# Performance work log

Hardware: AMD Instinct MI355X
Metric: run time of the kernel (lower is better)

## Reference

```python
import jax, jax.numpy as jnp
import numpy as np

N = 32768      # total nodes (512 graphs x 64 padded nodes)
E = 262144     # edges (avg degree 8)
F_IN = 74      # atom feature dim
D0 = 128       # dim_embedding
D1 = 256       # hidden feats
B = 512        # batch_size (graphs)
NPG = 64       # nodes per graph
EPS = 1e-5     # BatchNorm1d eps


def setup_inputs() -> dict:
    key = jax.random.key(0)
    ks = jax.random.split(key, 8)
    def rn(k, shape, s=0.05):
        return jax.random.normal(k, shape, jnp.float32) * s
    # init_transform weight [D0, F_IN]; padding=True zeroes the last row
    W_init = rn(ks[0], (D0, F_IN)).at[-1].set(0.0)
    return {
        "node_feats": jax.random.normal(ks[1], (N, F_IN), jnp.float32),
        "W_init": W_init,
        "gcn_w1": rn(ks[2], (D0, D1)), "gcn_b1": jnp.zeros((D1,), jnp.float32),
        "res_w1": rn(ks[3], (D1, D0)), "res_b1": jnp.zeros((D1,), jnp.float32),
        "bn_g1": jnp.ones((D1,), jnp.float32), "bn_b1": jnp.zeros((D1,), jnp.float32),
        "gcn_w2": rn(ks[4], (D1, D1)), "gcn_b2": jnp.zeros((D1,), jnp.float32),
        "bn_g2": jnp.ones((D1,), jnp.float32), "bn_b2": jnp.zeros((D1,), jnp.float32),
        "edge_src": jax.random.randint(ks[5], (E,), 0, N),
        "edge_dst": jax.random.randint(ks[6], (E,), 0, N),
    }


def _agg(x, src, dst):
    # DGL GraphConv norm='both': D_out^{-1/2} gather-scatter D_in^{-1/2}, degrees clamped to >= 1
    ones = jnp.ones((src.shape[0],), x.dtype)
    deg_out = jnp.clip(jax.ops.segment_sum(ones, src, num_segments=N), 1.0)
    deg_in = jnp.clip(jax.ops.segment_sum(ones, dst, num_segments=N), 1.0)
    xs = x * jax.lax.rsqrt(deg_out)[:, None]
    agg = jax.ops.segment_sum(xs[src], dst, num_segments=N)  # [N, d]
    return agg * jax.lax.rsqrt(deg_in)[:, None]


def _bn(x, g, b):
    # BatchNorm1d training-mode: batch stats over node axis, biased var
    m = x.mean(0)
    v = x.var(0)
    return (x - m) * jax.lax.rsqrt(v + EPS) * g + b


def reference(node_feats, W_init, gcn_w1, gcn_b1, res_w1, res_b1, bn_g1, bn_b1,
              gcn_w2, gcn_b2, bn_g2, bn_b2, edge_src, edge_dst):
    h = node_feats @ W_init.T  # [N, D0]
    # layer 1: residual Linear 128->256, GCN(aggregate then weight, since in<out), GELU, BN
    res = h @ res_w1.T + res_b1
    g = jax.nn.gelu(_agg(h, edge_src, edge_dst) @ gcn_w1 + gcn_b1, approximate=False)
    h = _bn(g + res, bn_g1, bn_b1)
    # layer 2: Identity residual
    g = jax.nn.gelu(_agg(h, edge_src, edge_dst) @ gcn_w2 + gcn_b2, approximate=False)
    h = _bn(g + h, bn_g2, bn_b2)
    return h.reshape(B, NPG, D1)
```

## Files before the change

kernel.cpp:

```cpp
#include <hip/hip_runtime.h>
#include <hip/hip_bf16.h>
#include <math.h>

#define N_NODES 32768
#define E_EDGES 262144
#define F_INF   74
#define KP      96
#define D0      128
#define D1      256
#define BN_EPS  1e-5f
#define RBLK    2048

typedef float f32x4 __attribute__((ext_vector_type(4)));
typedef short s16x8 __attribute__((ext_vector_type(8)));

__device__ __forceinline__ float b2f(ushort h) { return __uint_as_float(((unsigned)h) << 16); }
__device__ __forceinline__ ushort f2b(float f) {
    unsigned u = __float_as_uint(f);
    return (ushort)((u + 0x7FFFu + ((u >> 16) & 1u)) >> 16);
}
__device__ __forceinline__ float gelu_exact(float x) {
    return 0.5f * x * (1.0f + erff(x * 0.70710678118654752440f));
}


__global__ void k_front_a(const int* __restrict__ src, const int* __restrict__ dst,
                          int* __restrict__ deg,
                          const float* __restrict__ nf, const float* __restrict__ Wi,
                          const float* __restrict__ w1, const float* __restrict__ rw,
                          const float* __restrict__ w2,
                          ushort* __restrict__ nfB, ushort* __restrict__ WTB,
                          ushort* __restrict__ WB1, ushort* __restrict__ RWB,
                          ushort* __restrict__ WB2) {
    int bid = blockIdx.x;
    int tid = threadIdx.x;
    if (bid < 1024) {
        int e = bid * 256 + tid;
        atomicAdd(&deg[src[e]], 1);
        atomicAdd(&deg[N_NODES + dst[e]], 1);
        return;
    }
    int idx = (bid - 1024) * 256 + tid;
    {
        int n = idx / KP, k = idx - n * KP;
        nfB[idx] = (k < F_INF) ? f2b(nf[n * F_INF + k]) : (ushort)0;
    }
    if (idx < D0 * KP) {
        int c = idx / KP, k = idx - c * KP;
        WTB[idx] = (k < F_INF) ? f2b(Wi[c * F_INF + k]) : (ushort)0;
    }
    if (idx < D1 * D0) {
        int n = idx >> 7, k = idx & 127;
        WB1[idx] = f2b(w1[k * D1 + n]);
        RWB[idx] = f2b(rw[idx]);
    }
    if (idx < D1 * D1) {
        int n = idx >> 8, k = idx & 255;
        WB2[idx] = f2b(w2[k * D1 + n]);
    }
}

__global__ __launch_bounds__(1024) void k_scan(const int* __restrict__ deg,
                                               int* __restrict__ row_off,
                                               float* __restrict__ rsq_out,
                                               float* __restrict__ rsq_in,
                                               int* __restrict__ cursor) {
    __shared__ int part[1024];
    int t = threadIdx.x;
    int base = t * 32;
    int loc[32];
    int s = 0;
    #pragma unroll
    for (int i = 0; i < 32; i++) { loc[i] = s; s += deg[N_NODES + base + i]; }
    part[t] = s;
    #pragma unroll
    for (int i = 0; i < 32; i++) {
        int n = base + i;
        int d_o = deg[n];           if (d_o < 1) d_o = 1;
        int d_i = deg[N_NODES + n]; if (d_i < 1) d_i = 1;
        rsq_out[n] = 1.0f / sqrtf((float)d_o);
        rsq_in[n]  = 1.0f / sqrtf((float)d_i);
        cursor[n] = 0;
    }
    __syncthreads();
    for (int off = 1; off < 1024; off <<= 1) {
        int v = 0;
        if (t >= off) v = part[t - off];
        __syncthreads();
        if (t >= off) part[t] += v;
        __syncthreads();
    }
    int pre = (t == 0) ? 0 : part[t - 1];
    #pragma unroll
    for (int i = 0; i < 32; i++) row_off[base + i] = pre + loc[i];
    if (t == 1023) row_off[N_NODES] = part[1023];
}


__global__ __launch_bounds__(512) void k_front_b(
    const int* __restrict__ src, const int* __restrict__ dst,
    const int* __restrict__ row_off, const float* __restrict__ rsq_out,
    int* __restrict__ cursor, int* __restrict__ csr_src, float* __restrict__ esc,
    const ushort* __restrict__ nfB, const ushort* __restrict__ WTB,
    ushort* __restrict__ h0) {
    int bid = blockIdx.x;
    int tid = threadIdx.x;
    if (bid < 512) {
        int e = bid * 512 + tid;
        int d = dst[e];
        int s = src[e];
        int slot = atomicAdd(&cursor[d], 1);
        int pos = row_off[d] + slot;
        csr_src[pos] = s;
        esc[pos] = rsq_out[s];
        return;
    }
    int b2 = bid - 512;
    int w = tid >> 6, lane = tid & 63, m = lane & 15, g4 = lane >> 4;
    int col = w * 16 + m;
    int rbase = b2 * 16;
    s16x8 B[3], A[3];
    #pragma unroll
    for (int j = 0; j < 3; j++)
        B[j] = *reinterpret_cast<const s16x8*>(&WTB[(size_t)col * KP + j * 32 + g4 * 8]);
    #pragma unroll
    for (int j = 0; j < 3; j++)
        A[j] = *reinterpret_cast<const s16x8*>(&nfB[(size_t)(rbase + m) * KP + j * 32 + g4 * 8]);
    f32x4 acc = (f32x4){0.f, 0.f, 0.f, 0.f};
    #pragma unroll
    for (int j = 0; j < 3; j++)
        acc = __builtin_amdgcn_mfma_f32_16x16x32_bf16(A[j], B[j], acc, 0, 0, 0);
    #pragma unroll
    for (int r = 0; r < 4; r++)
        h0[(size_t)(rbase + g4 * 4 + r) * D0 + col] = f2b(acc[r]);
}


__global__ __launch_bounds__(512) void k_layer1f(
    const ushort* __restrict__ h0B, const float* __restrict__ rsq_in,
    const int* __restrict__ row_off, const int* __restrict__ csr_src,
    const float* __restrict__ esc,
    const ushort* __restrict__ WB1, const ushort* __restrict__ RWB,
    const float* __restrict__ b1, const float* __restrict__ rb,
    ushort* __restrict__ t1B, float* __restrict__ partials) {
    __shared__ ushort sA[16 * 128];
    int tid = threadIdx.x;
    int rbase = blockIdx.x * 16;
    {
        int nloc = tid >> 5;
        int half = (tid >> 4) & 1;
        int node = rbase + nloc;
        int f = (tid & 15) * 8;
        int beg = row_off[node], end = row_off[node + 1];
        float a[8];
        #pragma unroll
        for (int j = 0; j < 8; j++) a[j] = 0.f;
        int e = beg + half;
        for (; e + 6 < end; e += 8) {
            int s0 = csr_src[e], s1 = csr_src[e + 2], s2 = csr_src[e + 4], s3 = csr_src[e + 6];
            float c0 = esc[e], c1 = esc[e + 2], c2 = esc[e + 4], c3 = esc[e + 6];
            s16x8 v0 = *reinterpret_cast<const s16x8*>(&h0B[(size_t)s0 * D0 + f]);
            s16x8 v1 = *reinterpret_cast<const s16x8*>(&h0B[(size_t)s1 * D0 + f]);
            s16x8 v2 = *reinterpret_cast<const s16x8*>(&h0B[(size_t)s2 * D0 + f]);
            s16x8 v3 = *reinterpret_cast<const s16x8*>(&h0B[(size_t)s3 * D0 + f]);
            #pragma unroll
            for (int j = 0; j < 8; j++)
                a[j] += b2f((ushort)v0[j]) * c0 + b2f((ushort)v1[j]) * c1 +
                        b2f((ushort)v2[j]) * c2 + b2f((ushort)v3[j]) * c3;
        }
        for (; e < end; e += 2) {
            int s = csr_src[e];
            float sc = esc[e];
            s16x8 v = *reinterpret_cast<const s16x8*>(&h0B[(size_t)s * D0 + f]);
            #pragma unroll
            for (int j = 0; j < 8; j++) a[j] += b2f((ushort)v[j]) * sc;
        }
        #pragma unroll
        for (int j = 0; j < 8; j++) a[j] += __shfl_xor(a[j], 16);
        if (half == 0) {
            float si = rsq_in[node];
            s16x8 o;
            #pragma unroll
            for (int j = 0; j < 8; j++) o[j] = (short)f2b(a[j] * si);
            int boff = nloc * 256 + ((f * 2) ^ ((nloc & 15) << 4));
            *reinterpret_cast<s16x8*>(((char*)sA) + boff) = o;
        }
    }
    __syncthreads();
    int w = tid >> 6, lane = tid & 63, m = lane & 15, g4 = lane >> 4;
    int cb = w * 32;
    s16x8 BG[2][4], BR[2][4];
    #pragma unroll
    for (int nt = 0; nt < 2; nt++)
        #pragma unroll
        for (int j = 0; j < 4; j++) {
            BG[nt][j] = *reinterpret_cast<const s16x8*>(&WB1[(size_t)(cb + nt * 16 + m) * D0 + j * 32 + g4 * 8]);
            BR[nt][j] = *reinterpret_cast<const s16x8*>(&RWB[(size_t)(cb + nt * 16 + m) * D0 + j * 32 + g4 * 8]);
        }
    float bg[2], brv[2];
    #pragma unroll
    for (int nt = 0; nt < 2; nt++) {
        bg[nt]  = b1[cb + nt * 16 + m];
        brv[nt] = rb[cb + nt * 16 + m];
    }
    s16x8 aA[4], aH[4];
    #pragma unroll
    for (int j = 0; j < 4; j++) {
        int boff = m * 256 + (((j * 4 + g4) * 16) ^ ((m & 15) << 4));
        aA[j] = *reinterpret_cast<const s16x8*>(((const char*)sA) + boff);
        aH[j] = *reinterpret_cast<const s16x8*>(&h0B[(size_t)(rbase + m) * D0 + j * 32 + g4 * 8]);
    }
    f32x4 accG[2], accR[2];
    #pragma unroll
    for (int nt = 0; nt < 2; nt++) {
        accG[nt] = (f32x4){0.f, 0.f, 0.f, 0.f};
        accR[nt] = (f32x4){0.f, 0.f, 0.f, 0.f};
    }
    #pragma unroll
    for (int j = 0; j < 4; j++)
        #pragma unroll
        for (int nt = 0; nt < 2; nt++) {
            accG[nt] = __builtin_amdgcn_mfma_f32_16x16x32_bf16(aA[j], BG[nt][j], accG[nt], 0, 0, 0);
            accR[nt] = __builtin_amdgcn_mfma_f32_16x16x32_bf16(aH[j], BR[nt][j], accR[nt], 0, 0, 0);
        }
    float ps[2] = {0.f, 0.f}, pq[2] = {0.f, 0.f};
    #pragma unroll
    for (int nt = 0; nt < 2; nt++) {
        int col = cb + nt * 16 + m;
        #pragma unroll
        for (int r = 0; r < 4; r++) {
            int orow = rbase + g4 * 4 + r;
            float v = gelu_exact(accG[nt][r] + bg[nt]) + accR[nt][r] + brv[nt];
            t1B[(size_t)orow * D1 + col] = f2b(v);
            ps[nt] += v; pq[nt] += v * v;
        }
    }
    #pragma unroll
    for (int nt = 0; nt < 2; nt++) {
        float s = ps[nt], q = pq[nt];
        s += __shfl_xor(s, 16); s += __shfl_xor(s, 32);
        q += __shfl_xor(q, 16); q += __shfl_xor(q, 32);
        if (g4 == 0) {
            int col = cb + nt * 16 + m;
            partials[(size_t)col * RBLK + blockIdx.x] = s;
            partials[(size_t)(256 + col) * RBLK + blockIdx.x] = q;
        }
    }
}


__global__ __launch_bounds__(512) void k_layer2f(
    const ushort* __restrict__ t1B,
    const float* __restrict__ sc1, const float* __restrict__ sh1,
    const float* __restrict__ rsq_in,
    const int* __restrict__ row_off, const int* __restrict__ csr_src,
    const float* __restrict__ esc,
    const ushort* __restrict__ WB2, const float* __restrict__ b2,
    ushort* __restrict__ t2B, float* __restrict__ partials) {
    __shared__ ushort sA[16 * 256];
    int tid = threadIdx.x;
    int rbase = blockIdx.x * 16;
    {
        int nloc = tid >> 5;
        int half = (tid >> 4) & 1;
        int node = rbase + nloc;
        int f0 = (tid & 15) * 8;
        int beg = row_off[node], end = row_off[node + 1];
        float a0[8], a1[8];
        #pragma unroll
        for (int j = 0; j < 8; j++) { a0[j] = 0.f; a1[j] = 0.f; }
        float ssum = 0.f;
        int e = beg + half;
        for (; e + 6 < end; e += 8) {
            int s0 = csr_src[e], s1 = csr_src[e + 2], s2 = csr_src[e + 4], s3 = csr_src[e + 6];
            float c0 = esc[e], c1 = esc[e + 2], c2 = esc[e + 4], c3 = esc[e + 6];
            const s16x8* p0 = reinterpret_cast<const s16x8*>(&t1B[(size_t)s0 * D1 + f0]);
            const s16x8* p1 = reinterpret_cast<const s16x8*>(&t1B[(size_t)s1 * D1 + f0]);
            const s16x8* p2 = reinterpret_cast<const s16x8*>(&t1B[(size_t)s2 * D1 + f0]);
            const s16x8* p3 = reinterpret_cast<const s16x8*>(&t1B[(size_t)s3 * D1 + f0]);
            s16x8 v00 = p0[0], v01 = p0[16];
            s16x8 v10 = p1[0], v11 = p1[16];
            s16x8 v20 = p2[0], v21 = p2[16];
            s16x8 v30 = p3[0], v31 = p3[16];
            ssum += c0 + c1 + c2 + c3;
            #pragma unroll
            for (int j = 0; j < 8; j++) {
                a0[j] += b2f((ushort)v00[j]) * c0 + b2f((ushort)v10[j]) * c1 +
                         b2f((ushort)v20[j]) * c2 + b2f((ushort)v30[j]) * c3;
                a1[j] += b2f((ushort)v01[j]) * c0 + b2f((ushort)v11[j]) * c1 +
                         b2f((ushort)v21[j]) * c2 + b2f((ushort)v31[j]) * c3;
            }
        }
        for (; e < end; e += 2) {
            int s = csr_src[e];
            float sc = esc[e];
            const s16x8* p = reinterpret_cast<const s16x8*>(&t1B[(size_t)s * D1 + f0]);
            s16x8 v0 = p[0], v1 = p[16];
            ssum += sc;
            #pragma unroll
            for (int j = 0; j < 8; j++) {
                a0[j] += b2f((ushort)v0[j]) * sc;
                a1[j] += b2f((ushort)v1[j]) * sc;
            }
        }
        #pragma unroll
        for (int j = 0; j < 8; j++) {
            a0[j] += __shfl_xor(a0[j], 16);
            a1[j] += __shfl_xor(a1[j], 16);
        }
        ssum += __shfl_xor(ssum, 16);
        if (half == 0) {
            float si = rsq_in[node];
            s16x8 o0, o1;
            #pragma unroll
            for (int j = 0; j < 8; j++) {
                o0[j] = (short)f2b((sc1[f0 + j] * a0[j] + sh1[f0 + j] * ssum) * si);
                o1[j] = (short)f2b((sc1[f0 + 128 + j] * a1[j] + sh1[f0 + 128 + j] * ssum) * si);
            }
            int swz = (nloc & 15) << 4;
            int b0 = nloc * 512 + ((f0 * 2) ^ swz);
            int b1_ = nloc * 512 + (((f0 + 128) * 2) ^ swz);
            *reinterpret_cast<s16x8*>(((char*)sA) + b0) = o0;
            *reinterpret_cast<s16x8*>(((char*)sA) + b1_) = o1;
        }
    }
    __syncthreads();
    int w = tid >> 6, lane = tid & 63, m = lane & 15, g4 = lane >> 4;
    int cb = w * 32;
    ushort rres[2][4];
    #pragma unroll
    for (int nt = 0; nt < 2; nt++) {
        int col = cb + nt * 16 + m;
        #pragma unroll
        for (int r = 0; r < 4; r++)
            rres[nt][r] = t1B[(size_t)(rbase + g4 * 4 + r) * D1 + col];
    }
    s16x8 BG[2][8];
    #pragma unroll
    for (int nt = 0; nt < 2; nt++)
        #pragma unroll
        for (int j = 0; j < 8; j++)
            BG[nt][j] = *reinterpret_cast<const s16x8*>(&WB2[(size_t)(cb + nt * 16 + m) * D1 + j * 32 + g4 * 8]);
    float bg[2], a1c[2], s1c[2];
    #pragma unroll
    for (int nt = 0; nt < 2; nt++) {
        int col = cb + nt * 16 + m;
        bg[nt] = b2[col]; a1c[nt] = sc1[col]; s1c[nt] = sh1[col];
    }
    s16x8 aA[8];
    #pragma unroll
    for (int j = 0; j < 8; j++) {
        int boff = m * 512 + (((j * 4 + g4) * 16) ^ ((m & 15) << 4));
        aA[j] = *reinterpret_cast<const s16x8*>(((const char*)sA) + boff);
    }
    f32x4 acc[2];
    #pragma unroll
    for (int nt = 0; nt < 2; nt++) acc[nt] = (f32x4){0.f, 0.f, 0.f, 0.f};
    #pragma unroll
    for (int j = 0; j < 8; j++)
        #pragma unroll
        for (int nt = 0; nt < 2; nt++)
            acc[nt] = __builtin_amdgcn_mfma_f32_16x16x32_bf16(aA[j], BG[nt][j], acc[nt], 0, 0, 0);
    float ps[2] = {0.f, 0.f}, pq[2] = {0.f, 0.f};
    #pragma unroll
    for (int nt = 0; nt < 2; nt++) {
        int col = cb + nt * 16 + m;
        #pragma unroll
        for (int r = 0; r < 4; r++) {
            int orow = rbase + g4 * 4 + r;
            float h1v = fmaf(b2f(rres[nt][r]), a1c[nt], s1c[nt]);
            float v = gelu_exact(acc[nt][r] + bg[nt]) + h1v;
            t2B[(size_t)orow * D1 + col] = f2b(v);
            ps[nt] += v; pq[nt] += v * v;
        }
    }
    #pragma unroll
    for (int nt = 0; nt < 2; nt++) {
        float s = ps[nt], q = pq[nt];
        s += __shfl_xor(s, 16); s += __shfl_xor(s, 32);
        q += __shfl_xor(q, 16); q += __shfl_xor(q, 32);
        if (g4 == 0) {
            int col = cb + nt * 16 + m;
            partials[(size_t)col * RBLK + blockIdx.x] = s;
            partials[(size_t)(256 + col) * RBLK + blockIdx.x] = q;
        }
    }
}


__global__ __launch_bounds__(256) void k_reduce(
    const float* __restrict__ partials, const float* __restrict__ g,
    const float* __restrict__ b, float* __restrict__ sc, float* __restrict__ sh) {
    int c = blockIdx.x;
    int t = threadIdx.x;
    const float* ps = partials + (size_t)c * RBLK;
    const float* pq = partials + (size_t)(256 + c) * RBLK;
    float s = 0.f, q = 0.f;
    #pragma unroll
    for (int k = 0; k < 8; k++) { s += ps[t + 256 * k]; q += pq[t + 256 * k]; }
    __shared__ float Ls[256], Lq[256];
    Ls[t] = s; Lq[t] = q;
    __syncthreads();
    for (int o = 128; o > 0; o >>= 1) {
        if (t < o) { Ls[t] += Ls[t + o]; Lq[t] += Lq[t + o]; }
        __syncthreads();
    }
    if (t == 0) {
        float m = Ls[0] * (1.0f / (float)N_NODES);
        float var = Lq[0] * (1.0f / (float)N_NODES) - m * m;
        float a = g[c] / sqrtf(var + BN_EPS);
        sc[c] = a;
        sh[c] = b[c] - m * a;
    }
}


__global__ __launch_bounds__(256) void k_apply(
    const ushort* __restrict__ t2B, const float* __restrict__ sc,
    const float* __restrict__ sh, float* __restrict__ out) {
    int idx = blockIdx.x * 256 + threadIdx.x;
    size_t base = (size_t)idx * 8;
    int c = (int)(base & 255);
    s16x8 v = *reinterpret_cast<const s16x8*>(&t2B[base]);
    float4 o0, o1;
    o0.x = fmaf(b2f((ushort)v[0]), sc[c + 0], sh[c + 0]);
    o0.y = fmaf(b2f((ushort)v[1]), sc[c + 1], sh[c + 1]);
    o0.z = fmaf(b2f((ushort)v[2]), sc[c + 2], sh[c + 2]);
    o0.w = fmaf(b2f((ushort)v[3]), sc[c + 3], sh[c + 3]);
    o1.x = fmaf(b2f((ushort)v[4]), sc[c + 4], sh[c + 4]);
    o1.y = fmaf(b2f((ushort)v[5]), sc[c + 5], sh[c + 5]);
    o1.z = fmaf(b2f((ushort)v[6]), sc[c + 6], sh[c + 6]);
    o1.w = fmaf(b2f((ushort)v[7]), sc[c + 7], sh[c + 7]);
    *reinterpret_cast<float4*>(&out[base]) = o0;
    *reinterpret_cast<float4*>(&out[base + 4]) = o1;
}


static inline size_t align256(size_t x) { return (x + 255) & ~(size_t)255; }

extern "C" void kernel_launch(void* const* d_in, const int* in_sizes, int n_in,
                              void* d_out, int out_size, void* d_ws, size_t ws_size,
                              hipStream_t stream) {
    const float* node_feats = (const float*)d_in[0];
    const float* W_init     = (const float*)d_in[1];
    const float* gcn_w1     = (const float*)d_in[2];
    const float* gcn_b1     = (const float*)d_in[3];
    const float* res_w1     = (const float*)d_in[4];
    const float* res_b1     = (const float*)d_in[5];
    const float* bn_g1      = (const float*)d_in[6];
    const float* bn_b1      = (const float*)d_in[7];
    const float* gcn_w2     = (const float*)d_in[8];
    const float* gcn_b2     = (const float*)d_in[9];
    const float* bn_g2      = (const float*)d_in[10];
    const float* bn_b2      = (const float*)d_in[11];
    const int*   edge_src   = (const int*)d_in[12];
    const int*   edge_dst   = (const int*)d_in[13];
    float* out = (float*)d_out;

    char* p = (char*)d_ws;
    size_t off = 0;
    auto take = [&](size_t bytes) { void* r = p + off; off += align256(bytes); return r; };

    ushort* h0B   = (ushort*)take((size_t)N_NODES * D0 * 2);
    ushort* t1B   = (ushort*)take((size_t)N_NODES * D1 * 2);
    ushort* t2B   = (ushort*)take((size_t)N_NODES * D1 * 2);
    ushort* nfB   = (ushort*)take((size_t)N_NODES * KP * 2);
    ushort* WTB   = (ushort*)take((size_t)D0 * KP * 2);
    ushort* WB1   = (ushort*)take((size_t)D1 * D0 * 2);
    ushort* RWB   = (ushort*)take((size_t)D1 * D0 * 2);
    ushort* WB2   = (ushort*)take((size_t)D1 * D1 * 2);
    float*  part1 = (float*)take((size_t)2 * 256 * RBLK * 4);
    float*  part2 = (float*)take((size_t)2 * 256 * RBLK * 4);
    float*  sc1   = (float*)take(256 * 4);
    float*  sh1   = (float*)take(256 * 4);
    float*  sc2   = (float*)take(256 * 4);
    float*  sh2   = (float*)take(256 * 4);
    float*  rsq_out = (float*)take((size_t)N_NODES * 4);
    float*  rsq_in  = (float*)take((size_t)N_NODES * 4);
    int*    degi    = (int*)take((size_t)2 * N_NODES * 4);
    int*    cursor  = (int*)take((size_t)N_NODES * 4);
    int*    row_off = (int*)take((size_t)(N_NODES + 2) * 4);
    int*    csr_src = (int*)take((size_t)E_EDGES * 4);
    float*  esc     = (float*)take((size_t)E_EDGES * 4);

    hipMemsetAsync(degi, 0, (size_t)2 * N_NODES * 4, stream);

    k_front_a<<<1024 + (N_NODES * KP) / 256, 256, 0, stream>>>(
        edge_src, edge_dst, degi, node_feats, W_init, gcn_w1, res_w1, gcn_w2,
        nfB, WTB, WB1, RWB, WB2);

    k_scan<<<1, 1024, 0, stream>>>(degi, row_off, rsq_out, rsq_in, cursor);

    k_front_b<<<512 + N_NODES / 16, 512, 0, stream>>>(
        edge_src, edge_dst, row_off, rsq_out, cursor, csr_src, esc, nfB, WTB, h0B);

    k_layer1f<<<RBLK, 512, 0, stream>>>(h0B, rsq_in, row_off, csr_src, esc,
                                        WB1, RWB, gcn_b1, res_b1, t1B, part1);
    k_reduce<<<256, 256, 0, stream>>>(part1, bn_g1, bn_b1, sc1, sh1);

    k_layer2f<<<RBLK, 512, 0, stream>>>(t1B, sc1, sh1, rsq_in, row_off, csr_src, esc,
                                        WB2, gcn_b2, t2B, part2);
    k_reduce<<<256, 256, 0, stream>>>(part2, bn_g2, bn_b2, sc2, sh2);

    k_apply<<<(N_NODES * D1 / 8) / 256, 256, 0, stream>>>(t2B, sc2, sh2, out);
}
```

Baseline: 234.5 us.

## Double rows per block in fused GCN layer kernels with 1024-thread blocks

Each layer kernel block now handles 32 nodes with 1024 threads (16 waves), and each wave owns 16 output columns across two row tiles instead of 32 columns over one row tile. Weight fragments are loaded once per wave and reused across both row tiles. This halves the number of blocks and BN partial entries, and the reduce kernel is adjusted to sum 1024 partials. The intent is to cut weight reloads and per-block overhead, at the cost of larger blocks that may lower occupancy and scheduling flexibility.

```diff
diff --git a/kernel.cpp b/kernel.cpp
--- a/kernel.cpp
+++ b/kernel.cpp
@@ -9,7 +9,7 @@
 #define D0      128
 #define D1      256
 #define BN_EPS  1e-5f
-#define RBLK    2048
+#define RBLK    1024
 
 typedef float f32x4 __attribute__((ext_vector_type(4)));
 typedef short s16x8 __attribute__((ext_vector_type(8)));
@@ -136,16 +136,16 @@
 }
 
 
-__global__ __launch_bounds__(512) void k_layer1f(
+__global__ __launch_bounds__(1024) void k_layer1f(
     const ushort* __restrict__ h0B, const float* __restrict__ rsq_in,
     const int* __restrict__ row_off, const int* __restrict__ csr_src,
     const float* __restrict__ esc,
     const ushort* __restrict__ WB1, const ushort* __restrict__ RWB,
     const float* __restrict__ b1, const float* __restrict__ rb,
     ushort* __restrict__ t1B, float* __restrict__ partials) {
-    __shared__ ushort sA[16 * 128];
+    __shared__ ushort sA[32 * 128];
     int tid = threadIdx.x;
-    int rbase = blockIdx.x * 16;
+    int rbase = blockIdx.x * 32;
     {
         int nloc = tid >> 5;
         int half = (tid >> 4) & 1;
@@ -188,68 +188,50 @@
     }
     __syncthreads();
     int w = tid >> 6, lane = tid & 63, m = lane & 15, g4 = lane >> 4;
-    int cb = w * 32;
-    s16x8 BG[2][4], BR[2][4];
-    #pragma unroll
-    for (int nt = 0; nt < 2; nt++)
+    int col = w * 16 + m;
+    s16x8 BG[4], BR[4];
+    #pragma unroll
+    for (int j = 0; j < 4; j++) {
+        BG[j] = *reinterpret_cast<const s16x8*>(&WB1[(size_t)col * D0 + j * 32 + g4 * 8]);
+        BR[j] = *reinterpret_cast<const s16x8*>(&RWB[(size_t)col * D0 + j * 32 + g4 * 8]);
+    }
+    float bg = b1[col], brv = rb[col];
+    float ps = 0.f, pq = 0.f;
+    #pragma unroll
+    for (int rt = 0; rt < 2; rt++) {
+        int row = rt * 16 + m;
+        s16x8 aA[4], aH[4];
         #pragma unroll
         for (int j = 0; j < 4; j++) {
-            BG[nt][j] = *reinterpret_cast<const s16x8*>(&WB1[(size_t)(cb + nt * 16 + m) * D0 + j * 32 + g4 * 8]);
-            BR[nt][j] = *reinterpret_cast<const s16x8*>(&RWB[(size_t)(cb + nt * 16 + m) * D0 + j * 32 + g4 * 8]);
-        }
-    float bg[2], brv[2];
-    #pragma unroll
-    for (int nt = 0; nt < 2; nt++) {
-        bg[nt]  = b1[cb + nt * 16 + m];
-        brv[nt] = rb[cb + nt * 16 + m];
-    }
-    s16x8 aA[4], aH[4];
-    #pragma unroll
-    for (int j = 0; j < 4; j++) {
-        int boff = m * 256 + (((j * 4 + g4) * 16) ^ ((m & 15) << 4));
-        aA[j] = *reinterpret_cast<const s16x8*>(((const char*)sA) + boff);
-        aH[j] = *reinterpret_cast<const s16x8*>(&h0B[(size_t)(rbase + m) * D0 + j * 32 + g4 * 8]);
-    }
-    f32x4 accG[2], accR[2];
-    #pragma unroll
-    for (int nt = 0; nt < 2; nt++) {
-        accG[nt] = (f32x4){0.f, 0.f, 0.f, 0.f};
-        accR[nt] = (f32x4){0.f, 0.f, 0.f, 0.f};
-    }
-    #pragma unroll
-    for (int j = 0; j < 4; j++)
-        #pragma unroll
-        for (int nt = 0; nt < 2; nt++) {
-            accG[nt] = __builtin_amdgcn_mfma_f32_16x16x32_bf16(aA[j], BG[nt][j], accG[nt], 0, 0, 0);
-            accR[nt] = __builtin_amdgcn_mfma_f32_16x16x32_bf16(aH[j], BR[nt][j], accR[nt], 0, 0, 0);
-        }
-    float ps[2] = {0.f, 0.f}, pq[2] = {0.f, 0.f};
-    #pragma unroll
-    for (int nt = 0; nt < 2; nt++) {
-        int col = cb + nt * 16 + m;
+            int boff = row * 256 + (((j * 4 + g4) * 16) ^ ((row & 15) << 4));
+            aA[j] = *reinterpret_cast<const s16x8*>(((const char*)sA) + boff);
+            aH[j] = *reinterpret_cast<const s16x8*>(&h0B[(size_t)(rbase + row) * D0 + j * 32 + g4 * 8]);
+        }
+        f32x4 accG = (f32x4){0.f, 0.f, 0.f, 0.f};
+        f32x4 accR = (f32x4){0.f, 0.f, 0.f, 0.f};
+        #pragma unroll
+        for (int j = 0; j < 4; j++) {
+            accG = __builtin_amdgcn_mfma_f32_16x16x32_bf16(aA[j], BG[j], accG, 0, 0, 0);
+            accR = __builtin_amdgcn_mfma_f32_16x16x32_bf16(aH[j], BR[j], accR, 0, 0, 0);
+        }
         #pragma unroll
         for (int r = 0; r < 4; r++) {
-            int orow = rbase + g4 * 4 + r;
-            float v = gelu_exact(accG[nt][r] + bg[nt]) + accR[nt][r] + brv[nt];
+            int orow = rbase + rt * 16 + g4 * 4 + r;
+            float v = gelu_exact(accG[r] + bg) + accR[r] + brv;
             t1B[(size_t)orow * D1 + col] = f2b(v);
-            ps[nt] += v; pq[nt] += v * v;
-        }
-    }
-    #pragma unroll
-    for (int nt = 0; nt < 2; nt++) {
-        float s = ps[nt], q = pq[nt];
-        s += __shfl_xor(s, 16); s += __shfl_xor(s, 32);
-        q += __shfl_xor(q, 16); q += __shfl_xor(q, 32);
-        if (g4 == 0) {
-            int col = cb + nt * 16 + m;
-            partials[(size_t)col * RBLK + blockIdx.x] = s;
-            partials[(size_t)(256 + col) * RBLK + blockIdx.x] = q;
-        }
-    }
-}
-
-
-__global__ __launch_bounds__(512) void k_layer2f(
+            ps += v; pq += v * v;
+        }
+    }
+    ps += __shfl_xor(ps, 16); ps += __shfl_xor(ps, 32);
+    pq += __shfl_xor(pq, 16); pq += __shfl_xor(pq, 32);
+    if (g4 == 0) {
+        partials[(size_t)col * RBLK + blockIdx.x] = ps;
+        partials[(size_t)(256 + col) * RBLK + blockIdx.x] = pq;
+    }
+}
+
+
+__global__ __launch_bounds__(1024) void k_layer2f(
     const ushort* __restrict__ t1B,
     const float* __restrict__ sc1, const float* __restrict__ sh1,
     const float* __restrict__ rsq_in,
@@ -257,9 +239,9 @@
     const float* __restrict__ esc,
     const ushort* __restrict__ WB2, const float* __restrict__ b2,
     ushort* __restrict__ t2B, float* __restrict__ partials) {
-    __shared__ ushort sA[16 * 256];
+    __shared__ ushort sA[32 * 256];
     int tid = threadIdx.x;
-    int rbase = blockIdx.x * 16;
+    int rbase = blockIdx.x * 32;
     {
         int nloc = tid >> 5;
         int half = (tid >> 4) & 1;
@@ -326,64 +308,46 @@
     }
     __syncthreads();
     int w = tid >> 6, lane = tid & 63, m = lane & 15, g4 = lane >> 4;
-    int cb = w * 32;
+    int col = w * 16 + m;
     ushort rres[2][4];
     #pragma unroll
-    for (int nt = 0; nt < 2; nt++) {
-        int col = cb + nt * 16 + m;
+    for (int rt = 0; rt < 2; rt++)
         #pragma unroll
         for (int r = 0; r < 4; r++)
-            rres[nt][r] = t1B[(size_t)(rbase + g4 * 4 + r) * D1 + col];
-    }
-    s16x8 BG[2][8];
-    #pragma unroll
-    for (int nt = 0; nt < 2; nt++)
+            rres[rt][r] = t1B[(size_t)(rbase + rt * 16 + g4 * 4 + r) * D1 + col];
+    s16x8 BG[8];
+    #pragma unroll
+    for (int j = 0; j < 8; j++)
+        BG[j] = *reinterpret_cast<const s16x8*>(&WB2[(size_t)col * D1 + j * 32 + g4 * 8]);
+    float bg = b2[col], a1c = sc1[col], s1c = sh1[col];
+    float ps = 0.f, pq = 0.f;
+    #pragma unroll
+    for (int rt = 0; rt < 2; rt++) {
+        int row = rt * 16 + m;
+        s16x8 aA[8];
+        #pragma unroll
+        for (int j = 0; j < 8; j++) {
+            int boff = row * 512 + (((j * 4 + g4) * 16) ^ ((row & 15) << 4));
+            aA[j] = *reinterpret_cast<const s16x8*>(((const char*)sA) + boff);
+        }
+        f32x4 acc = (f32x4){0.f, 0.f, 0.f, 0.f};
         #pragma unroll
         for (int j = 0; j < 8; j++)
-            BG[nt][j] = *reinterpret_cast<const s16x8*>(&WB2[(size_t)(cb + nt * 16 + m) * D1 + j * 32 + g4 * 8]);
-    float bg[2], a1c[2], s1c[2];
-    #pragma unroll
-    for (int nt = 0; nt < 2; nt++) {
-        int col = cb + nt * 16 + m;
-        bg[nt] = b2[col]; a1c[nt] = sc1[col]; s1c[nt] = sh1[col];
-    }
-    s16x8 aA[8];
-    #pragma unroll
-    for (int j = 0; j < 8; j++) {
-        int boff = m * 512 + (((j * 4 + g4) * 16) ^ ((m & 15) << 4));
-        aA[j] = *reinterpret_cast<const s16x8*>(((const char*)sA) + boff);
-    }
-    f32x4 acc[2];
-    #pragma unroll
-    for (int nt = 0; nt < 2; nt++) acc[nt] = (f32x4){0.f, 0.f, 0.f, 0.f};
-    #pragma unroll
-    for (int j = 0; j < 8; j++)
-        #pragma unroll
-        for (int nt = 0; nt < 2; nt++)
-            acc[nt] = __builtin_amdgcn_mfma_f32_16x16x32_bf16(aA[j], BG[nt][j], acc[nt], 0, 0, 0);
-    float ps[2] = {0.f, 0.f}, pq[2] = {0.f, 0.f};
-    #pragma unroll
-    for (int nt = 0; nt < 2; nt++) {
-        int col = cb + nt * 16 + m;
+            acc = __builtin_amdgcn_mfma_f32_16x16x32_bf16(aA[j], BG[j], acc, 0, 0, 0);
         #pragma unroll
         for (int r = 0; r < 4; r++) {
-            int orow = rbase + g4 * 4 + r;
-            float h1v = fmaf(b2f(rres[nt][r]), a1c[nt], s1c[nt]);
-            float v = gelu_exact(acc[nt][r] + bg[nt]) + h1v;
+            int orow = rbase + rt * 16 + g4 * 4 + r;
+            float h1v = fmaf(b2f(rres[rt][r]), a1c, s1c);
+            float v = gelu_exact(acc[r] + bg) + h1v;
             t2B[(size_t)orow * D1 + col] = f2b(v);
-            ps[nt] += v; pq[nt] += v * v;
-        }
-    }
-    #pragma unroll
-    for (int nt = 0; nt < 2; nt++) {
-        float s = ps[nt], q = pq[nt];
-        s += __shfl_xor(s, 16); s += __shfl_xor(s, 32);
-        q += __shfl_xor(q, 16); q += __shfl_xor(q, 32);
-        if (g4 == 0) {
-            int col = cb + nt * 16 + m;
-            partials[(size_t)col * RBLK + blockIdx.x] = s;
-            partials[(size_t)(256 + col) * RBLK + blockIdx.x] = q;
-        }
+            ps += v; pq += v * v;
+        }
+    }
+    ps += __shfl_xor(ps, 16); ps += __shfl_xor(ps, 32);
+    pq += __shfl_xor(pq, 16); pq += __shfl_xor(pq, 32);
+    if (g4 == 0) {
+        partials[(size_t)col * RBLK + blockIdx.x] = ps;
+        partials[(size_t)(256 + col) * RBLK + blockIdx.x] = pq;
     }
 }
 
@@ -395,9 +359,8 @@
     int t = threadIdx.x;
     const float* ps = partials + (size_t)c * RBLK;
     const float* pq = partials + (size_t)(256 + c) * RBLK;
-    float s = 0.f, q = 0.f;
-    #pragma unroll
-    for (int k = 0; k < 8; k++) { s += ps[t + 256 * k]; q += pq[t + 256 * k]; }
+    float s = ps[t] + ps[t + 256] + ps[t + 512] + ps[t + 768];
+    float q = pq[t] + pq[t + 256] + pq[t + 512] + pq[t + 768];
     __shared__ float Ls[256], Lq[256];
     Ls[t] = s; Lq[t] = q;
     __syncthreads();
@@ -494,12 +457,12 @@
     k_front_b<<<512 + N_NODES / 16, 512, 0, stream>>>(
         edge_src, edge_dst, row_off, rsq_out, cursor, csr_src, esc, nfB, WTB, h0B);
 
-    k_layer1f<<<RBLK, 512, 0, stream>>>(h0B, rsq_in, row_off, csr_src, esc,
-                                        WB1, RWB, gcn_b1, res_b1, t1B, part1);
+    k_layer1f<<<RBLK, 1024, 0, stream>>>(h0B, rsq_in, row_off, csr_src, esc,
+                                         WB1, RWB, gcn_b1, res_b1, t1B, part1);
     k_reduce<<<256, 256, 0, stream>>>(part1, bn_g1, bn_b1, sc1, sh1);
 
-    k_layer2f<<<RBLK, 512, 0, stream>>>(t1B, sc1, sh1, rsq_in, row_off, csr_src, esc,
-                                        WB2, gcn_b2, t2B, part2);
+    k_layer2f<<<RBLK, 1024, 0, stream>>>(t1B, sc1, sh1, rsq_in, row_off, csr_src, esc,
+                                         WB2, gcn_b2, t2B, part2);
     k_reduce<<<256, 256, 0, stream>>>(part2, bn_g2, bn_b2, sc2, sh2);
 
     k_apply<<<(N_NODES * D1 / 8) / 256, 256, 0, stream>>>(t2B, sc2, sh2, out);
```

New measurement: 217.9 us. -7.1%, faster.
